# Optimization experiments

Hardware: AMD Instinct MI355X
Metric: run time of the kernel (lower is better)

The kernel has to match this reference:

```python
import jax, jax.numpy as jnp
import numpy as np

NODE_DIM = 64  # Net.node_dim


def _peg_conv(x, pos, edge_index, W, b, em_w, em_b):
    """PEGConv: GCN norm (with self-loops) + positional edge gate sigmoid(Linear(1,1)(sqdist))."""
    n = x.shape[0]
    loop = jnp.arange(n)
    row = jnp.concatenate([edge_index[0], loop])  # source j (with self-loops)
    col = jnp.concatenate([edge_index[1], loop])  # target i
    ones = jnp.ones(row.shape[0], dtype=x.dtype)
    deg = jax.ops.segment_sum(ones, col, num_segments=n)
    dinv = jnp.where(deg > 0, jax.lax.rsqrt(deg), 0.0)
    norm = dinv[row] * dinv[col]                                       # [E+N]
    h = x @ W                                                          # [N, out]
    sq = jnp.sum((pos[col] - pos[row]) ** 2, axis=-1, keepdims=True)   # [E+N, 1]
    gate = jax.nn.sigmoid(sq * em_w[0, 0] + em_b[0])                   # edge MLP Linear(1,1)+Sigmoid
    msg = gate * (norm[:, None] * h[row])                              # [E+N, out]
    return jax.ops.segment_sum(msg, col, num_segments=n) + b


def setup_inputs() -> dict:
    key = jax.random.key(0)
    ks = jax.random.split(key, 12)
    N, E_MP, E_LP = 50000, 800000, 100000
    IN, POS, HID = 128, 32, 64
    return {
        "x": jax.random.normal(ks[0], (N, IN), jnp.float32),
        "pos": jax.random.normal(ks[1], (N, POS), jnp.float32),
        "pos_edge_index": jax.random.randint(ks[2], (2, E_LP), 0, N),
        "neg_edge_index": jax.random.randint(ks[3], (2, E_LP), 0, N),
        "train_pos": jax.random.randint(ks[4], (2, E_MP), 0, N),
        "W1": jax.random.normal(ks[5], (IN, HID), jnp.float32) / np.float32(np.sqrt(IN)),
        "b1": jnp.zeros((HID,), jnp.float32),
        "em1_w": jax.random.normal(ks[6], (1, 1), jnp.float32),
        "em1_b": jnp.zeros((1,), jnp.float32),
        "W2": jax.random.normal(ks[7], (HID, HID), jnp.float32) / np.float32(np.sqrt(HID)),
        "b2": jnp.zeros((HID,), jnp.float32),
        "em2_w": jax.random.normal(ks[8], (1, 1), jnp.float32),
        "em2_b": jnp.zeros((1,), jnp.float32),
        "fc_w": jax.random.normal(ks[9], (1, 2), jnp.float32),  # nn.Linear(2,1) weight
        "fc_b": jnp.zeros((1,), jnp.float32),
    }


def reference(x, pos, pos_edge_index, neg_edge_index, train_pos,
              W1, b1, em1_w, em1_b, W2, b2, em2_w, em2_b, fc_w, fc_b):
    edge_index = jnp.concatenate([pos_edge_index, neg_edge_index], axis=-1)  # [2, 2*E_LP]
    h = _peg_conv(x, pos, train_pos, W1, b1, em1_w, em1_b)
    h = _peg_conv(h, pos, train_pos, W2, b2, em2_w, em2_b)
    nodes_first = h[edge_index[0], :NODE_DIM]
    nodes_second = h[edge_index[1], :NODE_DIM]
    pe = jnp.sum((pos[edge_index[0]] - pos[edge_index[1]]) ** 2, axis=-1, keepdims=True)
    pred = jnp.sum(nodes_first * nodes_second, axis=-1, keepdims=True)
    feats = jnp.concatenate([pred, pe], axis=1)  # [2*E_LP, 2]
    return feats @ fc_w.T + fc_b                 # [2*E_LP, 1]
```

## Files before the change

### kernel.cpp

```cpp
#include <hip/hip_runtime.h>
#include <hip/hip_fp16.h>

#define HID 64
#define POS_DIM 32
#define IN_DIM 128

using short8 = __attribute__((ext_vector_type(8))) short;
using f32x4  = __attribute__((ext_vector_type(4))) float;

__device__ __forceinline__ float fsig(float v) {
    return 1.0f / (1.0f + __expf(-v));
}

__device__ __forceinline__ unsigned short f2bf(float f) {
    unsigned int u = __float_as_uint(f);
    u = u + 0x7FFFu + ((u >> 16) & 1u);
    return (unsigned short)(u >> 16);
}
__device__ __forceinline__ float bf2f(unsigned short s) {
    return __uint_as_float(((unsigned int)s) << 16);
}
__device__ __forceinline__ float2 bfpair(unsigned int u) {
    return make_float2(__uint_as_float(u << 16),
                       __uint_as_float(u & 0xFFFF0000u));
}
__device__ __forceinline__ unsigned int pack2bf(float a, float b) {
    return (unsigned int)f2bf(a) | ((unsigned int)f2bf(b) << 16);
}
__device__ __forceinline__ int pack2h(float a, float b) {
    __half2 h2 = __floats2half2_rn(a, b);
    return *reinterpret_cast<int*>(&h2);
}
__device__ __forceinline__ float cextract(int bits, int layer) {
    __half2 h2 = *reinterpret_cast<__half2*>(&bits);
    return layer ? __half2float(__high2half(h2)) : __half2float(__low2half(h2));
}

__global__ __launch_bounds__(256) void k_posbf(const float* __restrict__ pos,
                                               unsigned int* __restrict__ posh,
                                               int total2) {
    int i = blockIdx.x * blockDim.x + threadIdx.x;
    if (i >= total2) return;
    float2 v = ((const float2*)pos)[i];
    posh[i] = pack2bf(v.x, v.y);
}

__global__ __launch_bounds__(256) void k_hist(const int* __restrict__ tp,
                                              int* cnt, int E) {
    int i = blockIdx.x * blockDim.x + threadIdx.x;
    if (i < E) atomicAdd(&cnt[tp[E + i]], 1);
}

__global__ __launch_bounds__(256) void k_bsum(const int* __restrict__ cnt,
                                              int* __restrict__ bsum, int n) {
    int i = blockIdx.x * 256 + threadIdx.x;
    int v = (i < n) ? cnt[i] : 0;
    #pragma unroll
    for (int o = 32; o; o >>= 1) v += __shfl_down(v, o);
    __shared__ int w[4];
    int lane = threadIdx.x & 63, wid = threadIdx.x >> 6;
    if (lane == 0) w[wid] = v;
    __syncthreads();
    if (threadIdx.x == 0) bsum[blockIdx.x] = w[0] + w[1] + w[2] + w[3];
}

__global__ __launch_bounds__(256) void k_scan2(const int* __restrict__ cnt,
                                               const int* __restrict__ bsum,
                                               int* __restrict__ off,
                                               int* __restrict__ cur,
                                               float* __restrict__ dinv,
                                               int n, int Etot) {
    __shared__ int s[256];
    __shared__ int wsum[4];
    int tid = threadIdx.x, bid = blockIdx.x;
    int p = 0;
    for (int t = tid; t < bid; t += 256) p += bsum[t];
    #pragma unroll
    for (int o = 32; o; o >>= 1) p += __shfl_down(p, o);
    int lane = tid & 63, wid = tid >> 6;
    if (lane == 0) wsum[wid] = p;
    __syncthreads();
    int bpre = wsum[0] + wsum[1] + wsum[2] + wsum[3];
    int i = bid * 256 + tid;
    int v = (i < n) ? cnt[i] : 0;
    s[tid] = v;
    __syncthreads();
    #pragma unroll
    for (int d = 1; d < 256; d <<= 1) {
        int t_ = (tid >= d) ? s[tid - d] : 0;
        __syncthreads();
        s[tid] += t_;
        __syncthreads();
    }
    if (i < n) {
        int ov = bpre + s[tid] - v;
        off[i]  = ov;
        cur[i]  = ov;
        dinv[i] = rsqrtf((float)(v + 1));
    }
    if (i == 0) off[n] = Etot;
}

__global__ __launch_bounds__(256) void k_fill2(const int* __restrict__ tp,
                                               const unsigned int* __restrict__ posh,
                                               const float* __restrict__ dinv,
                                               int* cur,
                                               const float* em1w, const float* em1b,
                                               const float* em2w, const float* em2b,
                                               int2* __restrict__ csr, int E) {
    int lane = threadIdx.x & 63;
    int wid  = threadIdx.x >> 6;
    int sub  = lane >> 3;
    int j    = lane & 7;
    int base = (blockIdx.x * 4 + wid) * 16;
    int e0 = base + sub;
    int e1 = base + 8 + sub;
    if (e0 >= E) return;
    bool v1 = (e1 < E);
    int row0 = tp[e0],            col0 = tp[E + e0];
    int row1 = v1 ? tp[e1] : 0;
    int col1 = v1 ? tp[E + e1] : 0;
    const uint2* ph = (const uint2*)posh;
    uint2 a0 = ph[(size_t)row0 * 8 + j];
    uint2 b0 = ph[(size_t)col0 * 8 + j];
    uint2 a1 = ph[(size_t)row1 * 8 + j];
    uint2 b1 = ph[(size_t)col1 * 8 + j];
    float s0, s1;
    {
        float2 ax = bfpair(a0.x), ay = bfpair(a0.y);
        float2 bx = bfpair(b0.x), by = bfpair(b0.y);
        float d0 = ax.x - bx.x, d1 = ax.y - bx.y;
        float d2 = ay.x - by.x, d3 = ay.y - by.y;
        s0 = d0 * d0;
        s0 = fmaf(d1, d1, s0); s0 = fmaf(d2, d2, s0); s0 = fmaf(d3, d3, s0);
    }
    {
        float2 ax = bfpair(a1.x), ay = bfpair(a1.y);
        float2 bx = bfpair(b1.x), by = bfpair(b1.y);
        float d0 = ax.x - bx.x, d1 = ax.y - bx.y;
        float d2 = ay.x - by.x, d3 = ay.y - by.y;
        s1 = d0 * d0;
        s1 = fmaf(d1, d1, s1); s1 = fmaf(d2, d2, s1); s1 = fmaf(d3, d3, s1);
    }
    s0 += __shfl_xor(s0, 1);  s1 += __shfl_xor(s1, 1);
    s0 += __shfl_xor(s0, 2);  s1 += __shfl_xor(s1, 2);
    s0 += __shfl_xor(s0, 4);  s1 += __shfl_xor(s1, 4);
    if (j < 2) {
        bool valid = j ? v1 : true;
        if (valid) {
            int   rr = j ? row1 : row0;
            int   cc = j ? col1 : col0;
            float ss = j ? s1   : s0;
            float nrm = dinv[rr] * dinv[cc];
            float c1 = fsig(ss * em1w[0] + em1b[0]) * nrm;
            float c2 = fsig(ss * em2w[0] + em2b[0]) * nrm;
            int slot = atomicAdd(&cur[cc], 1);
            csr[slot] = make_int2(rr, pack2h(c1, c2));
        }
    }
}

template<int K, bool IN_BF16>
__global__ __launch_bounds__(256) void k_gemm_mfma(const void* __restrict__ Xv,
                                                   const float* __restrict__ W,
                                                   unsigned short* __restrict__ H,
                                                   int n) {
    constexpr int RB   = K * 2;
    constexpr int CPR  = K / 8;
    __shared__ unsigned char lds[64 * RB * 2];
    unsigned char* As = lds;
    unsigned char* Bt = lds + 64 * RB;

    int tid  = threadIdx.x;
    int row0 = blockIdx.x * 64;

    for (int i = tid; i < 64 * CPR; i += 256) {
        int r  = i / CPR;
        int kb = i % CPR;
        uint4 val;
        if (row0 + r < n) {
            if (IN_BF16) {
                val = *(const uint4*)((const unsigned short*)Xv + (size_t)(row0 + r) * K + kb * 8);
            } else {
                const float* src = (const float*)Xv + (size_t)(row0 + r) * K + kb * 8;
                float4 f0 = ((const float4*)src)[0];
                float4 f1 = ((const float4*)src)[1];
                val.x = pack2bf(f0.x, f0.y); val.y = pack2bf(f0.z, f0.w);
                val.z = pack2bf(f1.x, f1.y); val.w = pack2bf(f1.z, f1.w);
            }
        } else {
            val = make_uint4(0, 0, 0, 0);
        }
        *(uint4*)(As + r * RB + ((kb ^ (r & 7)) << 4)) = val;
    }
    for (int i = tid; i < K * 16; i += 256) {
        int k  = i / 16;
        int c0 = (i % 16) * 4;
        float4 w = ((const float4*)W)[i];
        #pragma unroll
        for (int u = 0; u < 4; ++u) {
            int c = c0 + u;
            float vv = (u == 0) ? w.x : (u == 1) ? w.y : (u == 2) ? w.z : w.w;
            int byte = c * RB + ((((k * 2) >> 4) ^ (c & 7)) << 4) + ((k & 7) * 2);
            *(unsigned short*)(Bt + byte) = f2bf(vv);
        }
    }
    __syncthreads();

    int wv   = tid >> 6;
    int lane = tid & 63;
    int l15  = lane & 15;
    int g    = lane >> 4;

    f32x4 acc[4] = {{0,0,0,0},{0,0,0,0},{0,0,0,0},{0,0,0,0}};
    #pragma unroll
    for (int kk = 0; kk < K / 32; ++kk) {
        int kc = kk * 4 + g;
        int arow = wv * 16 + l15;
        short8 a = *(const short8*)(As + arow * RB + ((kc ^ (arow & 7)) << 4));
        #pragma unroll
        for (int cb = 0; cb < 4; ++cb) {
            int c = cb * 16 + l15;
            short8 b = *(const short8*)(Bt + c * RB + ((kc ^ (c & 7)) << 4));
            acc[cb] = __builtin_amdgcn_mfma_f32_16x16x32_bf16(a, b, acc[cb], 0, 0, 0);
        }
    }

    #pragma unroll
    for (int cb = 0; cb < 4; ++cb) {
        #pragma unroll
        for (int r = 0; r < 4; ++r) {
            int row = row0 + wv * 16 + g * 4 + r;
            if (row < n) H[(size_t)row * HID + cb * 16 + l15] = f2bf(acc[cb][r]);
        }
    }
}

__global__ __launch_bounds__(256) void k_agg(const int* __restrict__ off,
                                             const int2* __restrict__ csr,
                                             const unsigned short* __restrict__ h,
                                             const float* __restrict__ dinv,
                                             const float* __restrict__ bias,
                                             const float* emb,
                                             unsigned short* __restrict__ out,
                                             int n, int layer) {
    int wid  = threadIdx.x >> 6;
    int lane = threadIdx.x & 63;
    int half = lane >> 5;
    int q    = lane & 31;
    int i = blockIdx.x * 4 + wid;
    if (i >= n) return;
    float accx = 0.0f, accy = 0.0f;
    if (half == 0) {
        float di = dinv[i];
        float sc = fsig(emb[0]) * di * di;
        float2 bv = ((const float2*)bias)[q];
        float2 hv = bfpair(((const unsigned int*)(h + (size_t)i * HID))[q]);
        accx = fmaf(sc, hv.x, bv.x);
        accy = fmaf(sc, hv.y, bv.y);
    }
    int s  = off[i] + half;
    int s1 = off[i + 1];
    for (; s + 6 < s1; s += 8) {
        int2 ea = csr[s],     eb = csr[s + 2];
        int2 ec = csr[s + 4], ed = csr[s + 6];
        float ca = cextract(ea.y, layer);
        float cb = cextract(eb.y, layer);
        float cc = cextract(ec.y, layer);
        float cd = cextract(ed.y, layer);
        float2 va = bfpair(((const unsigned int*)(h + (size_t)ea.x * HID))[q]);
        float2 vb = bfpair(((const unsigned int*)(h + (size_t)eb.x * HID))[q]);
        float2 vc = bfpair(((const unsigned int*)(h + (size_t)ec.x * HID))[q]);
        float2 vd = bfpair(((const unsigned int*)(h + (size_t)ed.x * HID))[q]);
        accx = fmaf(ca, va.x, accx); accy = fmaf(ca, va.y, accy);
        accx = fmaf(cb, vb.x, accx); accy = fmaf(cb, vb.y, accy);
        accx = fmaf(cc, vc.x, accx); accy = fmaf(cc, vc.y, accy);
        accx = fmaf(cd, vd.x, accx); accy = fmaf(cd, vd.y, accy);
    }
    for (; s < s1; s += 2) {
        int2 ea = csr[s];
        float ca = cextract(ea.y, layer);
        float2 va = bfpair(((const unsigned int*)(h + (size_t)ea.x * HID))[q]);
        accx = fmaf(ca, va.x, accx); accy = fmaf(ca, va.y, accy);
    }
    accx += __shfl_down(accx, 32);
    accy += __shfl_down(accy, 32);
    if (half == 0)
        ((unsigned int*)out)[(size_t)i * (HID / 2) + q] = pack2bf(accx, accy);
}

__global__ __launch_bounds__(256) void k_predict(const int* __restrict__ pei,
                                                 const int* __restrict__ nei,
                                                 const unsigned short* __restrict__ h,
                                                 const float* __restrict__ pos,
                                                 const float* fcw, const float* fcb,
                                                 float* __restrict__ out, int Elp) {
    int j = threadIdx.x & 7;
    int e = blockIdx.x * 32 + (threadIdx.x >> 3);
    if (e >= 2 * Elp) return;
    int src, dst;
    if (e < Elp) { src = pei[e];        dst = pei[Elp + e]; }
    else         { src = nei[e - Elp];  dst = nei[e];       }
    uint4 hs = ((const uint4*)(h + (size_t)src * HID))[j];
    uint4 hd = ((const uint4*)(h + (size_t)dst * HID))[j];
    float p = 0.0f;
    {
        float2 a, b;
        a = bfpair(hs.x); b = bfpair(hd.x);
        p = fmaf(a.x, b.x, p); p = fmaf(a.y, b.y, p);
        a = bfpair(hs.y); b = bfpair(hd.y);
        p = fmaf(a.x, b.x, p); p = fmaf(a.y, b.y, p);
        a = bfpair(hs.z); b = bfpair(hd.z);
        p = fmaf(a.x, b.x, p); p = fmaf(a.y, b.y, p);
        a = bfpair(hs.w); b = bfpair(hd.w);
        p = fmaf(a.x, b.x, p); p = fmaf(a.y, b.y, p);
    }
    float4 pa = ((const float4*)(pos + (size_t)src * POS_DIM))[j];
    float4 pb = ((const float4*)(pos + (size_t)dst * POS_DIM))[j];
    float dx = pa.x - pb.x, dy = pa.y - pb.y, dz = pa.z - pb.z, dw = pa.w - pb.w;
    float pe = 0.0f;
    pe = fmaf(dx, dx, pe); pe = fmaf(dy, dy, pe);
    pe = fmaf(dz, dz, pe); pe = fmaf(dw, dw, pe);
    p  += __shfl_xor(p, 1);  pe += __shfl_xor(pe, 1);
    p  += __shfl_xor(p, 2);  pe += __shfl_xor(pe, 2);
    p  += __shfl_xor(p, 4);  pe += __shfl_xor(pe, 4);
    if (j == 0) out[e] = fcw[0] * p + fcw[1] * pe + fcb[0];
}

static inline size_t align16(size_t v) { return (v + 15) & ~(size_t)15; }

extern "C" void kernel_launch(void* const* d_in, const int* in_sizes, int n_in,
                              void* d_out, int out_size, void* d_ws, size_t ws_size,
                              hipStream_t stream) {
    const float* x    = (const float*)d_in[0];
    const float* pos  = (const float*)d_in[1];
    const int*   pei  = (const int*)d_in[2];
    const int*   nei  = (const int*)d_in[3];
    const int*   tp   = (const int*)d_in[4];
    const float* W1   = (const float*)d_in[5];
    const float* b1   = (const float*)d_in[6];
    const float* em1w = (const float*)d_in[7];
    const float* em1b = (const float*)d_in[8];
    const float* W2   = (const float*)d_in[9];
    const float* b2   = (const float*)d_in[10];
    const float* em2w = (const float*)d_in[11];
    const float* em2b = (const float*)d_in[12];
    const float* fcw  = (const float*)d_in[13];
    const float* fcb  = (const float*)d_in[14];
    float* outp = (float*)d_out;

    const int N   = in_sizes[0] / IN_DIM;
    const int E   = in_sizes[4] / 2;
    const int Elp = in_sizes[2] / 2;
    const int NB  = (N + 255) / 256;

    char* base = (char*)d_ws;
    size_t o = 0;
    int2* csr = (int2*)(base + o);                        o += align16((size_t)E * 8);
    int*   cnt  = (int*)(base + o);                       o += align16((size_t)N * 4);
    int*   off  = (int*)(base + o);                       o += align16((size_t)(N + 1) * 4);
    int*   cur  = (int*)(base + o);                       o += align16((size_t)N * 4);
    int*   bsum = (int*)(base + o);                       o += align16((size_t)NB * 4);
    float* dinv = (float*)(base + o);                     o += align16((size_t)N * 4);
    unsigned int* posh = (unsigned int*)(base + o);       o += align16((size_t)N * POS_DIM * 2);
    unsigned short* hbuf = (unsigned short*)(base + o);   o += align16((size_t)N * HID * 2);
    unsigned short* obuf = (unsigned short*)(base + o);   o += align16((size_t)N * HID * 2);

    hipMemsetAsync(cnt, 0, (size_t)N * 4, stream);
    k_posbf<<<(N * POS_DIM / 2 + 255) / 256, 256, 0, stream>>>(pos, posh, N * POS_DIM / 2);
    k_hist<<<(E + 255) / 256, 256, 0, stream>>>(tp, cnt, E);
    k_bsum<<<NB, 256, 0, stream>>>(cnt, bsum, N);
    k_scan2<<<NB, 256, 0, stream>>>(cnt, bsum, off, cur, dinv, N, E);
    k_fill2<<<(E + 63) / 64, 256, 0, stream>>>(tp, posh, dinv, cur,
                                               em1w, em1b, em2w, em2b, csr, E);

    k_gemm_mfma<IN_DIM, false><<<(N + 63) / 64, 256, 0, stream>>>(x, W1, hbuf, N);
    k_agg<<<(N + 3) / 4, 256, 0, stream>>>(off, csr, hbuf, dinv, b1, em1b, obuf, N, 0);

    k_gemm_mfma<HID, true><<<(N + 63) / 64, 256, 0, stream>>>(obuf, W2, hbuf, N);
    k_agg<<<(N + 3) / 4, 256, 0, stream>>>(off, csr, hbuf, dinv, b2, em2b, obuf, N, 1);

    k_predict<<<(2 * Elp + 31) / 32, 256, 0, stream>>>(pei, nei, obuf,
                                                       pos, fcw, fcb, outp, Elp);
}
```

Before: 197.5 us.

## Merge pos conversion with histogram and split aggregation into four edge lanes

The pos-to-bf16 conversion and the degree histogram are fused into one launch to save a kernel launch. The aggregation kernel is remapped so each wavefront handles four edges at once, with 16 lanes per edge each loading 8 bytes (4 bf16 features), instead of two edges with 32 lanes loading 4 bytes each. Partial sums are combined with xor shuffles across the four lane groups. This is meant to raise memory-level parallelism and load width in the gather, at the cost of extra shuffle reductions and more idle lanes on low-degree nodes.

```diff
diff --git a/kernel.cpp b/kernel.cpp
--- a/kernel.cpp
+++ b/kernel.cpp
@@ -36,18 +36,15 @@
     return layer ? __half2float(__high2half(h2)) : __half2float(__low2half(h2));
 }
 
-__global__ __launch_bounds__(256) void k_posbf(const float* __restrict__ pos,
-                                               unsigned int* __restrict__ posh,
-                                               int total2) {
+__global__ __launch_bounds__(256) void k_prep(const float* __restrict__ pos,
+                                              unsigned int* __restrict__ posh,
+                                              const int* __restrict__ tp,
+                                              int* cnt, int total2, int E) {
     int i = blockIdx.x * blockDim.x + threadIdx.x;
-    if (i >= total2) return;
-    float2 v = ((const float2*)pos)[i];
-    posh[i] = pack2bf(v.x, v.y);
-}
-
-__global__ __launch_bounds__(256) void k_hist(const int* __restrict__ tp,
-                                              int* cnt, int E) {
-    int i = blockIdx.x * blockDim.x + threadIdx.x;
+    if (i < total2) {
+        float2 v = ((const float2*)pos)[i];
+        posh[i] = pack2bf(v.x, v.y);
+    }
     if (i < E) atomicAdd(&cnt[tp[E + i]], 1);
 }
 
@@ -246,47 +243,70 @@
                                              int n, int layer) {
     int wid  = threadIdx.x >> 6;
     int lane = threadIdx.x & 63;
-    int half = lane >> 5;
-    int q    = lane & 31;
+    int q    = lane >> 4;
+    int t    = lane & 15;
     int i = blockIdx.x * 4 + wid;
     if (i >= n) return;
-    float accx = 0.0f, accy = 0.0f;
-    if (half == 0) {
+    const uint2* hrow = (const uint2*)h;
+    float4 acc = make_float4(0.f, 0.f, 0.f, 0.f);
+    if (q == 0) {
         float di = dinv[i];
         float sc = fsig(emb[0]) * di * di;
-        float2 bv = ((const float2*)bias)[q];
-        float2 hv = bfpair(((const unsigned int*)(h + (size_t)i * HID))[q]);
-        accx = fmaf(sc, hv.x, bv.x);
-        accy = fmaf(sc, hv.y, bv.y);
-    }
-    int s  = off[i] + half;
-    int s1 = off[i + 1];
-    for (; s + 6 < s1; s += 8) {
-        int2 ea = csr[s],     eb = csr[s + 2];
-        int2 ec = csr[s + 4], ed = csr[s + 6];
+        float4 bv = ((const float4*)bias)[t];
+        uint2 hv = hrow[(size_t)i * 16 + t];
+        float2 h0 = bfpair(hv.x), h1 = bfpair(hv.y);
+        acc.x = fmaf(sc, h0.x, bv.x);
+        acc.y = fmaf(sc, h0.y, bv.y);
+        acc.z = fmaf(sc, h1.x, bv.z);
+        acc.w = fmaf(sc, h1.y, bv.w);
+    }
+    int s0 = off[i], s1 = off[i + 1];
+    int s = s0;
+    for (; s + 15 < s1; s += 16) {
+        int2 ea = csr[s + q];
+        int2 eb = csr[s + q + 4];
+        int2 ec = csr[s + q + 8];
+        int2 ed = csr[s + q + 12];
         float ca = cextract(ea.y, layer);
         float cb = cextract(eb.y, layer);
         float cc = cextract(ec.y, layer);
         float cd = cextract(ed.y, layer);
-        float2 va = bfpair(((const unsigned int*)(h + (size_t)ea.x * HID))[q]);
-        float2 vb = bfpair(((const unsigned int*)(h + (size_t)eb.x * HID))[q]);
-        float2 vc = bfpair(((const unsigned int*)(h + (size_t)ec.x * HID))[q]);
-        float2 vd = bfpair(((const unsigned int*)(h + (size_t)ed.x * HID))[q]);
-        accx = fmaf(ca, va.x, accx); accy = fmaf(ca, va.y, accy);
-        accx = fmaf(cb, vb.x, accx); accy = fmaf(cb, vb.y, accy);
-        accx = fmaf(cc, vc.x, accx); accy = fmaf(cc, vc.y, accy);
-        accx = fmaf(cd, vd.x, accx); accy = fmaf(cd, vd.y, accy);
-    }
-    for (; s < s1; s += 2) {
-        int2 ea = csr[s];
+        uint2 va = hrow[(size_t)ea.x * 16 + t];
+        uint2 vb = hrow[(size_t)eb.x * 16 + t];
+        uint2 vc = hrow[(size_t)ec.x * 16 + t];
+        uint2 vd = hrow[(size_t)ed.x * 16 + t];
+        float2 p0, p1;
+        p0 = bfpair(va.x); p1 = bfpair(va.y);
+        acc.x = fmaf(ca, p0.x, acc.x); acc.y = fmaf(ca, p0.y, acc.y);
+        acc.z = fmaf(ca, p1.x, acc.z); acc.w = fmaf(ca, p1.y, acc.w);
+        p0 = bfpair(vb.x); p1 = bfpair(vb.y);
+        acc.x = fmaf(cb, p0.x, acc.x); acc.y = fmaf(cb, p0.y, acc.y);
+        acc.z = fmaf(cb, p1.x, acc.z); acc.w = fmaf(cb, p1.y, acc.w);
+        p0 = bfpair(vc.x); p1 = bfpair(vc.y);
+        acc.x = fmaf(cc, p0.x, acc.x); acc.y = fmaf(cc, p0.y, acc.y);
+        acc.z = fmaf(cc, p1.x, acc.z); acc.w = fmaf(cc, p1.y, acc.w);
+        p0 = bfpair(vd.x); p1 = bfpair(vd.y);
+        acc.x = fmaf(cd, p0.x, acc.x); acc.y = fmaf(cd, p0.y, acc.y);
+        acc.z = fmaf(cd, p1.x, acc.z); acc.w = fmaf(cd, p1.y, acc.w);
+    }
+    for (int u = s + q; u < s1; u += 4) {
+        int2 ea = csr[u];
         float ca = cextract(ea.y, layer);
-        float2 va = bfpair(((const unsigned int*)(h + (size_t)ea.x * HID))[q]);
-        accx = fmaf(ca, va.x, accx); accy = fmaf(ca, va.y, accy);
-    }
-    accx += __shfl_down(accx, 32);
-    accy += __shfl_down(accy, 32);
-    if (half == 0)
-        ((unsigned int*)out)[(size_t)i * (HID / 2) + q] = pack2bf(accx, accy);
+        uint2 va = hrow[(size_t)ea.x * 16 + t];
+        float2 p0 = bfpair(va.x), p1 = bfpair(va.y);
+        acc.x = fmaf(ca, p0.x, acc.x); acc.y = fmaf(ca, p0.y, acc.y);
+        acc.z = fmaf(ca, p1.x, acc.z); acc.w = fmaf(ca, p1.y, acc.w);
+    }
+    acc.x += __shfl_xor(acc.x, 16); acc.y += __shfl_xor(acc.y, 16);
+    acc.z += __shfl_xor(acc.z, 16); acc.w += __shfl_xor(acc.w, 16);
+    acc.x += __shfl_xor(acc.x, 32); acc.y += __shfl_xor(acc.y, 32);
+    acc.z += __shfl_xor(acc.z, 32); acc.w += __shfl_xor(acc.w, 32);
+    if (q == 0) {
+        uint2 o;
+        o.x = pack2bf(acc.x, acc.y);
+        o.y = pack2bf(acc.z, acc.w);
+        ((uint2*)out)[(size_t)i * 16 + t] = o;
+    }
 }
 
 __global__ __launch_bounds__(256) void k_predict(const int* __restrict__ pei,
@@ -366,9 +386,11 @@
     unsigned short* hbuf = (unsigned short*)(base + o);   o += align16((size_t)N * HID * 2);
     unsigned short* obuf = (unsigned short*)(base + o);   o += align16((size_t)N * HID * 2);
 
+    const int total2 = N * POS_DIM / 2;
+    const int prepN  = (total2 > E ? total2 : E);
+
     hipMemsetAsync(cnt, 0, (size_t)N * 4, stream);
-    k_posbf<<<(N * POS_DIM / 2 + 255) / 256, 256, 0, stream>>>(pos, posh, N * POS_DIM / 2);
-    k_hist<<<(E + 255) / 256, 256, 0, stream>>>(tp, cnt, E);
+    k_prep<<<(prepN + 255) / 256, 256, 0, stream>>>(pos, posh, tp, cnt, total2, E);
     k_bsum<<<NB, 256, 0, stream>>>(cnt, bsum, N);
     k_scan2<<<NB, 256, 0, stream>>>(cnt, bsum, off, cur, dinv, N, E);
     k_fill2<<<(E + 63) / 64, 256, 0, stream>>>(tp, posh, dinv, cur,
```

Result: faster. 189.2 us (-4.2%).
